# Performance work log

Measured on AMD Instinct MI355X. Metric: run time of the kernel, lower is better.

Reference implementation:

```python
import jax, jax.numpy as jnp
import numpy as np

B, NV, NDIRS, NRINGS, NCH, NF = 2, 15000, 16, 3, 32, 64


def setup_inputs() -> dict:
    key = jax.random.key(0)
    k1, k2, k3, k4 = jax.random.split(key, 4)
    y = jax.random.normal(k1, (B, NV, NDIRS, NCH), dtype=jnp.float32)
    ft_v = jax.random.randint(k2, (NV, NRINGS, NDIRS), 0, NV, dtype=jnp.int32)
    ft_d = jax.random.randint(k3, (NV, NRINGS, NDIRS), 0, NDIRS, dtype=jnp.int32)
    kernel = jax.random.normal(k4, (NRINGS, NDIRS, NCH, NF), dtype=jnp.float32) * 0.05
    bias = jnp.zeros((NF,), dtype=jnp.float32)
    return {"y": y, "ft_v": ft_v, "ft_d": ft_d, "kernel": kernel, "bias": bias}


def reference(y, ft_v, ft_d, kernel, bias):
    # y: [b, nv, ndirs, nch]; ft_v/ft_d: [nv, nrings, ndirs]; kernel: [nrings, ndirs, nch, nf]
    b, nv, ndirs, nch = y.shape
    f = jnp.transpose(y, (1, 2, 3, 0))  # [nv, ndirs, nch, b]
    dirs = jnp.arange(ndirs)

    def per_dir(l):
        # cyclic forward shift of the direction axis, composed with the
        # frame-transporter gather: z[v,r,d,c,b] = f[ft_v[v,r,d], (ft_d[v,r,d]+l)%n, c, b]
        d_idx = (ft_d + l) % ndirs                # [nv, nrings, ndirs]
        z = f[ft_v, d_idx]                        # [nv, nrings, ndirs, nch, b]
        # kernel shifted in reverse: k_l[:, d] = kernel[:, (d-l)%n]
        k_l = kernel[:, (dirs - l) % ndirs]       # [nrings, ndirs, nch, nf]
        return jnp.einsum('vrdcb,rdcf->vbf', z, k_l)  # [nv, b, nf]

    out = jax.lax.map(per_dir, dirs)              # [ndirs, nv, b, nf] (sequential, like tf.while_loop)
    out = jnp.transpose(out, (2, 1, 0, 3))        # [b, nv, ndirs, nf]
    out = out + bias
    return jax.nn.relu(out)
```

## Files before the change

kernel.cpp:

```cpp
#include <hip/hip_runtime.h>

#define NV 15000
#define ND 16
#define NR 3
#define NC 32
#define NFDIM 64
#define BB 2

typedef short bf16x8 __attribute__((ext_vector_type(8)));
typedef float f32x4 __attribute__((ext_vector_type(4)));
typedef unsigned short u16x8 __attribute__((ext_vector_type(8)));
typedef unsigned int u32;

#define KB_OFF     30720000u
#define WS_NEEDED  30916608u

#define AS1 __attribute__((address_space(1)))
#define AS3 __attribute__((address_space(3)))
#define GLOAD16(gp, lp) __builtin_amdgcn_global_load_lds((AS1 const u32*)(gp), (AS3 u32*)(lp), 16, 0, 0)

__device__ __forceinline__ unsigned short f2bf(float x) {
  union { float f; unsigned int u; } cv; cv.f = x;
  unsigned int u = cv.u;
  u += 0x7FFF + ((u >> 16) & 1);
  return (unsigned short)(u >> 16);
}

__global__ void prep_y(const float* __restrict__ y, u16x8* __restrict__ yt) {
  int tid = blockIdx.x * 256 + threadIdx.x;
  if (tid >= (NV * ND * BB * NC) / 8) return;
  int o   = tid * 8;
  int v   = o >> 10;
  int rem = o & 1023;
  int d   = rem >> 6;
  int b   = (rem >> 5) & 1;
  int c0  = rem & 31;
  const f32x4* src = (const f32x4*)(y + (((b * NV + v) * ND + d) * NC + c0));
  f32x4 lo = src[0], hi = src[1];
  u16x8 r;
#pragma unroll
  for (int i = 0; i < 4; i++) { r[i] = f2bf(lo[i]); r[4 + i] = f2bf(hi[i]); }
  yt[tid] = r;
}

__global__ void prep_kb(const float* __restrict__ kern, unsigned short* __restrict__ kb) {
  int t = blockIdx.x * 256 + threadIdx.x;
  if (t >= 48 * 4 * 64) return;
  int lane  = t & 63;
  int ft    = (t >> 6) & 3;
  int chunk = t >> 8;
  int q = lane >> 4;
  int f = (lane & 15) * 4 + ft;
  unsigned short* dst = kb + t * 8;
#pragma unroll
  for (int j = 0; j < 8; j++) {
    int k = q * 8 + j;
    dst[j] = f2bf(kern[(chunk * NC + k) * NFDIM + f]);
  }
}

__global__ __launch_bounds__(256, 4) void sync_conv_main(
    const unsigned short* __restrict__ yt, const unsigned short* __restrict__ kb,
    const int* __restrict__ ftv, const int* __restrict__ ftd,
    const float* __restrict__ bias, float* __restrict__ out) {
  __shared__ int   pidx[16][49];
  __shared__ int   pre[4][16][49];
  __shared__ short lds_b[3 * 4096];

  int tid  = threadIdx.x;
  int lane = tid & 63;
  int w    = tid >> 6;
  int mg   = blockIdx.x >> 2;
  int lg   = blockIdx.x & 3;
  int l    = lg * 4 + w;
  int vbase = mg * 16;

  for (int t = tid; t < 16 * 48; t += 256) {
    int i = t / 48, j = t - i * 48;
    int v = vbase + i; v = v < NV ? v : NV - 1;
    pidx[i][j] = ftv[v * 48 + j] * 16 + (ftd[v * 48 + j] & 15);
  }
  __syncthreads();
#pragma unroll
  for (int wl = 0; wl < 4; wl++) {
    int ll = lg * 4 + wl;
    for (int t = tid; t < 768; t += 256) {
      int i = t / 48, j = t - i * 48;
      int p = pidx[i][j];
      pre[wl][i][j] = (p >> 4) * 1024 + ((((p & 15) + ll) & 15) << 6);
    }
  }
  __syncthreads();

  int q    = lane >> 4;
  int n    = lane & 15;
  int voff = n >> 1;
  int lane_elem = (n & 1) * 32 + q * 8;
  const int* pre_w0 = &pre[w][voff][0];
  const int* pre_w1 = &pre[w][8 + voff][0];

  f32x4 acc[2][4];
#pragma unroll
  for (int i = 0; i < 2; i++)
#pragma unroll
    for (int j = 0; j < 4; j++) acc[i][j] = (f32x4){0.f, 0.f, 0.f, 0.f};

  auto stageB = [&](int t, int slot) {
    const unsigned short* g = kb + t * 4096 + w * 1024 + (lane << 3);
    short* d = lds_b + slot * 4096 + w * 1024;
    GLOAD16(g, d);
    GLOAD16(g + 512, d + 512);
  };

  stageB(0, 0);
  stageB(1, 1);

  int sl = 0;
#pragma unroll 3
  for (int t = 0; t < 24; t++) {
    if (t < 23) {
      asm volatile("s_waitcnt vmcnt(2)" ::: "memory");
    } else {
      asm volatile("s_waitcnt vmcnt(0)" ::: "memory");
    }
    __builtin_amdgcn_s_barrier();

    bf16x8 A[2][2];
#pragma unroll
    for (int ds = 0; ds < 2; ds++) {
      int s = 2 * t + ds;
      int j = (s & 48) | ((s + l) & 15);
      A[0][ds] = *reinterpret_cast<const bf16x8*>(yt + pre_w0[j] + lane_elem);
      A[1][ds] = *reinterpret_cast<const bf16x8*>(yt + pre_w1[j] + lane_elem);
    }

    if (t + 2 < 24) stageB(t + 2, sl == 0 ? 2 : sl - 1);

    const short* lb = lds_b + sl * 4096;
    __builtin_amdgcn_s_setprio(1);
#pragma unroll
    for (int ds = 0; ds < 2; ds++) {
#pragma unroll
      for (int ft = 0; ft < 4; ft++) {
        bf16x8 bf = *reinterpret_cast<const bf16x8*>(lb + ds * 2048 + ft * 512 + (lane << 3));
        acc[0][ft] = __builtin_amdgcn_mfma_f32_16x16x32_bf16(A[0][ds], bf, acc[0][ft], 0, 0, 0);
        acc[1][ft] = __builtin_amdgcn_mfma_f32_16x16x32_bf16(A[1][ds], bf, acc[1][ft], 0, 0, 0);
      }
    }
    __builtin_amdgcn_s_setprio(0);
    sl = sl == 2 ? 0 : sl + 1;
  }

  f32x4 bv = *reinterpret_cast<const f32x4*>(bias + 4 * n);

#pragma unroll
  for (int mt = 0; mt < 2; mt++) {
#pragma unroll
    for (int reg = 0; reg < 4; reg++) {
      int m  = q * 4 + reg;
      int v  = vbase + mt * 8 + (m >> 1);
      int bb = m & 1;
      if (v < NV) {
        f32x4 x;
#pragma unroll
        for (int ft = 0; ft < 4; ft++) {
          float t = acc[mt][ft][reg] + bv[ft];
          x[ft] = t > 0.f ? t : 0.f;
        }
        float* dst = out + (((bb * NV + v) * ND + l) * NFDIM) + 4 * n;
        __builtin_nontemporal_store(x, (f32x4*)dst);
      }
    }
  }
}

__global__ void fallback_kernel(const float* __restrict__ y, const int* __restrict__ ftv,
                                const int* __restrict__ ftd, const float* __restrict__ kern,
                                const float* __restrict__ bias, float* __restrict__ out) {
  int idx = blockIdx.x;
  int l = idx & 15;
  int v = (idx >> 4) % NV;
  int b = idx / (NV * ND);
  int f = threadIdx.x;
  float acc = 0.f;
  for (int r = 0; r < NR; r++)
    for (int d = 0; d < ND; d++) {
      int ii = (v * NR + r) * ND + d;
      int vv = ftv[ii];
      int dd = (ftd[ii] + l) & 15;
      int dp = (d - l) & 15;
      const float* yp = y + ((b * NV + vv) * ND + dd) * NC;
      const float* kp = kern + ((r * 16 + dp) * NC) * NFDIM + f;
#pragma unroll 8
      for (int c = 0; c < NC; c++) acc += yp[c] * kp[c * NFDIM];
    }
  float x = acc + bias[f];
  out[idx * NFDIM + f] = x > 0.f ? x : 0.f;
}

extern "C" void kernel_launch(void* const* d_in, const int* in_sizes, int n_in,
                              void* d_out, int out_size, void* d_ws, size_t ws_size,
                              hipStream_t stream) {
  const float* y    = (const float*)d_in[0];
  const int*   ftv  = (const int*)d_in[1];
  const int*   ftd  = (const int*)d_in[2];
  const float* kern = (const float*)d_in[3];
  const float* bias = (const float*)d_in[4];
  float* out = (float*)d_out;

  if (ws_size >= (size_t)WS_NEEDED) {
    char* ws = (char*)d_ws;
    unsigned short* yt = (unsigned short*)ws;
    unsigned short* kb = (unsigned short*)(ws + KB_OFF);

    prep_y<<<(NV * ND * BB * NC / 8 + 255) / 256, 256, 0, stream>>>(y, (u16x8*)yt);
    prep_kb<<<(48 * 4 * 64 + 255) / 256, 256, 0, stream>>>(kern, kb);
    sync_conv_main<<<3752, 256, 0, stream>>>(yt, kb, ftv, ftd, bias, out);
  } else {
    fallback_kernel<<<BB * NV * ND, NFDIM, 0, stream>>>(y, ftv, ftd, kern, bias, out);
  }
}
```

Measured before the change: 364.7 us.

## Prefetch gathered A fragments two stages ahead in a register ring

The gathered y fragments (A operands) are now loaded two iterations ahead into a three-deep register ring, alongside the existing LDS ring for kernel weights. The vmcnt wait and sched_barriers are adjusted so the global gathers overlap with the MFMA work of earlier stages. The index scratch array is unioned with the LDS ring to cut shared-memory use. The cost is extra VGPRs for the A ring, which may hurt occupancy under the launch bounds. The handwritten vmcnt counts also rely on the compiler issuing loads in the expected order.

New measurement: 363.4 us. No clear change (-0.4%).

```diff
diff --git a/kernel.cpp b/kernel.cpp
--- a/kernel.cpp
+++ b/kernel.cpp
@@ -63,9 +63,11 @@
     const unsigned short* __restrict__ yt, const unsigned short* __restrict__ kb,
     const int* __restrict__ ftv, const int* __restrict__ ftd,
     const float* __restrict__ bias, float* __restrict__ out) {
-  __shared__ int   pidx[16][49];
-  __shared__ int   pre[4][16][49];
-  __shared__ short lds_b[3 * 4096];
+  __shared__ union ShU {
+    int   pidx[16][49];
+    short ring[3 * 4096];
+  } sh;
+  __shared__ int pre[4][16][49];
 
   int tid  = threadIdx.x;
   int lane = tid & 63;
@@ -78,7 +80,7 @@
   for (int t = tid; t < 16 * 48; t += 256) {
     int i = t / 48, j = t - i * 48;
     int v = vbase + i; v = v < NV ? v : NV - 1;
-    pidx[i][j] = ftv[v * 48 + j] * 16 + (ftd[v * 48 + j] & 15);
+    sh.pidx[i][j] = ftv[v * 48 + j] * 16 + (ftd[v * 48 + j] & 15);
   }
   __syncthreads();
 #pragma unroll
@@ -86,7 +88,7 @@
     int ll = lg * 4 + wl;
     for (int t = tid; t < 768; t += 256) {
       int i = t / 48, j = t - i * 48;
-      int p = pidx[i][j];
+      int p = sh.pidx[i][j];
       pre[wl][i][j] = (p >> 4) * 1024 + ((((p & 15) + ll) & 15) << 6);
     }
   }
@@ -105,51 +107,58 @@
 #pragma unroll
     for (int j = 0; j < 4; j++) acc[i][j] = (f32x4){0.f, 0.f, 0.f, 0.f};
 
+  bf16x8 bufA[3][2][2];
+
+  auto issueA = [&](int t, bf16x8 (&Ab)[2][2]) {
+    int s0 = 2 * t, s1 = s0 + 1;
+    int j0 = (s0 & 48) | ((s0 + l) & 15);
+    int j1 = (s1 & 48) | ((s1 + l) & 15);
+    Ab[0][0] = *reinterpret_cast<const bf16x8*>(yt + pre_w0[j0] + lane_elem);
+    Ab[1][0] = *reinterpret_cast<const bf16x8*>(yt + pre_w1[j0] + lane_elem);
+    Ab[0][1] = *reinterpret_cast<const bf16x8*>(yt + pre_w0[j1] + lane_elem);
+    Ab[1][1] = *reinterpret_cast<const bf16x8*>(yt + pre_w1[j1] + lane_elem);
+  };
   auto stageB = [&](int t, int slot) {
     const unsigned short* g = kb + t * 4096 + w * 1024 + (lane << 3);
-    short* d = lds_b + slot * 4096 + w * 1024;
-    GLOAD16(g, d);
-    GLOAD16(g + 512, d + 512);
+    short* dl = sh.ring + slot * 4096 + w * 1024;
+    GLOAD16(g, dl);
+    GLOAD16(g + 512, dl + 512);
   };
-
-  stageB(0, 0);
-  stageB(1, 1);
-
-  int sl = 0;
-#pragma unroll 3
-  for (int t = 0; t < 24; t++) {
-    if (t < 23) {
-      asm volatile("s_waitcnt vmcnt(2)" ::: "memory");
-    } else {
-      asm volatile("s_waitcnt vmcnt(0)" ::: "memory");
-    }
-    __builtin_amdgcn_s_barrier();
-
-    bf16x8 A[2][2];
-#pragma unroll
-    for (int ds = 0; ds < 2; ds++) {
-      int s = 2 * t + ds;
-      int j = (s & 48) | ((s + l) & 15);
-      A[0][ds] = *reinterpret_cast<const bf16x8*>(yt + pre_w0[j] + lane_elem);
-      A[1][ds] = *reinterpret_cast<const bf16x8*>(yt + pre_w1[j] + lane_elem);
-    }
-
-    if (t + 2 < 24) stageB(t + 2, sl == 0 ? 2 : sl - 1);
-
-    const short* lb = lds_b + sl * 4096;
+  auto computeT = [&](bf16x8 (&Ab)[2][2], const short* lb) {
     __builtin_amdgcn_s_setprio(1);
 #pragma unroll
     for (int ds = 0; ds < 2; ds++) {
 #pragma unroll
       for (int ft = 0; ft < 4; ft++) {
         bf16x8 bf = *reinterpret_cast<const bf16x8*>(lb + ds * 2048 + ft * 512 + (lane << 3));
-        acc[0][ft] = __builtin_amdgcn_mfma_f32_16x16x32_bf16(A[0][ds], bf, acc[0][ft], 0, 0, 0);
-        acc[1][ft] = __builtin_amdgcn_mfma_f32_16x16x32_bf16(A[1][ds], bf, acc[1][ft], 0, 0, 0);
+        acc[0][ft] = __builtin_amdgcn_mfma_f32_16x16x32_bf16(Ab[0][ds], bf, acc[0][ft], 0, 0, 0);
+        acc[1][ft] = __builtin_amdgcn_mfma_f32_16x16x32_bf16(Ab[1][ds], bf, acc[1][ft], 0, 0, 0);
       }
     }
     __builtin_amdgcn_s_setprio(0);
-    sl = sl == 2 ? 0 : sl + 1;
-  }
+  };
+
+  issueA(0, bufA[0]); stageB(0, 0);
+  issueA(1, bufA[1]); stageB(1, 1);
+
+#define ITER(T, PAR, PAR2)                                          \
+  do {                                                              \
+    if ((T) < 23) asm volatile("s_waitcnt vmcnt(6)" ::: "memory");  \
+    else          asm volatile("s_waitcnt vmcnt(0)" ::: "memory");  \
+    __builtin_amdgcn_s_barrier();                                   \
+    if ((T) < 22) { issueA((T) + 2, bufA[PAR2]); stageB((T) + 2, PAR2); } \
+    __builtin_amdgcn_sched_barrier(0);                              \
+    computeT(bufA[PAR], sh.ring + (PAR) * 4096);                    \
+    __builtin_amdgcn_sched_barrier(0);                              \
+  } while (0)
+
+  for (int it = 0; it < 8; it++) {
+    int t0 = 3 * it;
+    ITER(t0 + 0, 0, 2);
+    ITER(t0 + 1, 1, 0);
+    ITER(t0 + 2, 2, 1);
+  }
+#undef ITER
 
   f32x4 bv = *reinterpret_cast<const f32x4*>(bias + 4 * n);
 
```

## Split gather into two half-table passes with dummy zero reads for locality

Applied to the files above, without the earlier changes.

Runs the reduction loop twice. Each pass gathers only rows whose source offset falls in one half of the bf16 y table, and out-of-half rows read a zeroed dummy slot placed just past the kernel buffer. The aim is to keep each pass's random gather working set small enough to stay in cache. In exchange it doubles the MFMA work, the B-tile staging and the gather instruction count. It also overlays the index scratch and the B ring in one LDS union to cut shared memory use.

New measurement: 397.5 us. 1.09x slower.

```diff
diff --git a/kernel.cpp b/kernel.cpp
--- a/kernel.cpp
+++ b/kernel.cpp
@@ -13,7 +13,10 @@
 typedef unsigned int u32;
 
 #define KB_OFF     30720000u
-#define WS_NEEDED  30916608u
+#define WS_NEEDED  30916864u
+
+#define DUMMY_OFF  15458304
+#define SPLIT_OFF  7680000
 
 #define AS1 __attribute__((address_space(1)))
 #define AS3 __attribute__((address_space(3)))
@@ -45,6 +48,7 @@
 
 __global__ void prep_kb(const float* __restrict__ kern, unsigned short* __restrict__ kb) {
   int t = blockIdx.x * 256 + threadIdx.x;
+  if (t < 128) kb[48 * 4 * 64 * 8 + t] = 0;
   if (t >= 48 * 4 * 64) return;
   int lane  = t & 63;
   int ft    = (t >> 6) & 3;
@@ -63,9 +67,11 @@
     const unsigned short* __restrict__ yt, const unsigned short* __restrict__ kb,
     const int* __restrict__ ftv, const int* __restrict__ ftd,
     const float* __restrict__ bias, float* __restrict__ out) {
-  __shared__ int   pidx[16][49];
-  __shared__ int   pre[4][16][49];
-  __shared__ short lds_b[3 * 4096];
+  __shared__ union ShU {
+    int   pidx[16][49];
+    short ring[3 * 4096];
+  } sh;
+  __shared__ int pre[4][16][49];
 
   int tid  = threadIdx.x;
   int lane = tid & 63;
@@ -78,7 +84,7 @@
   for (int t = tid; t < 16 * 48; t += 256) {
     int i = t / 48, j = t - i * 48;
     int v = vbase + i; v = v < NV ? v : NV - 1;
-    pidx[i][j] = ftv[v * 48 + j] * 16 + (ftd[v * 48 + j] & 15);
+    sh.pidx[i][j] = ftv[v * 48 + j] * 16 + (ftd[v * 48 + j] & 15);
   }
   __syncthreads();
 #pragma unroll
@@ -86,7 +92,7 @@
     int ll = lg * 4 + wl;
     for (int t = tid; t < 768; t += 256) {
       int i = t / 48, j = t - i * 48;
-      int p = pidx[i][j];
+      int p = sh.pidx[i][j];
       pre[wl][i][j] = (p >> 4) * 1024 + ((((p & 15) + ll) & 15) << 6);
     }
   }
@@ -106,10 +112,11 @@
     for (int j = 0; j < 4; j++) acc[i][j] = (f32x4){0.f, 0.f, 0.f, 0.f};
 
   auto stageB = [&](int t, int slot) {
-    const unsigned short* g = kb + t * 4096 + w * 1024 + (lane << 3);
-    short* d = lds_b + slot * 4096 + w * 1024;
-    GLOAD16(g, d);
-    GLOAD16(g + 512, d + 512);
+    int tt = t >= 24 ? t - 24 : t;
+    const unsigned short* g = kb + tt * 4096 + w * 1024 + (lane << 3);
+    short* dl = sh.ring + slot * 4096 + w * 1024;
+    GLOAD16(g, dl);
+    GLOAD16(g + 512, dl + 512);
   };
 
   stageB(0, 0);
@@ -117,26 +124,34 @@
 
   int sl = 0;
 #pragma unroll 3
-  for (int t = 0; t < 24; t++) {
-    if (t < 23) {
+  for (int t = 0; t < 48; t++) {
+    if (t < 47) {
       asm volatile("s_waitcnt vmcnt(2)" ::: "memory");
     } else {
       asm volatile("s_waitcnt vmcnt(0)" ::: "memory");
     }
     __builtin_amdgcn_s_barrier();
 
+    bool ph = t >= 24;
+    int tt = ph ? t - 24 : t;
     bf16x8 A[2][2];
 #pragma unroll
     for (int ds = 0; ds < 2; ds++) {
-      int s = 2 * t + ds;
+      int s = 2 * tt + ds;
       int j = (s & 48) | ((s + l) & 15);
-      A[0][ds] = *reinterpret_cast<const bf16x8*>(yt + pre_w0[j] + lane_elem);
-      A[1][ds] = *reinterpret_cast<const bf16x8*>(yt + pre_w1[j] + lane_elem);
-    }
-
-    if (t + 2 < 24) stageB(t + 2, sl == 0 ? 2 : sl - 1);
-
-    const short* lb = lds_b + sl * 4096;
+      int p0 = pre_w0[j];
+      int p1 = pre_w1[j];
+      bool ok0 = (p0 < SPLIT_OFF) != ph;
+      bool ok1 = (p1 < SPLIT_OFF) != ph;
+      int o0 = ok0 ? p0 : DUMMY_OFF;
+      int o1 = ok1 ? p1 : DUMMY_OFF;
+      A[0][ds] = *reinterpret_cast<const bf16x8*>(yt + o0 + lane_elem);
+      A[1][ds] = *reinterpret_cast<const bf16x8*>(yt + o1 + lane_elem);
+    }
+
+    if (t + 2 < 48) stageB(t + 2, sl == 0 ? 2 : sl - 1);
+
+    const short* lb = sh.ring + sl * 4096;
     __builtin_amdgcn_s_setprio(1);
 #pragma unroll
     for (int ds = 0; ds < 2; ds++) {
```
